# Optimization experiments

Hardware: AMD Instinct MI355X
Metric: run time of the kernel (lower is better)

Reference implementation:

```python
import jax, jax.numpy as jnp
import numpy as np

B, S, D, H = 32, 512, 512, 8
DH = D // H
EXP_FF, EXP_CONV, K = 4, 2, 31
EPS = 1e-5


def _layernorm(x, g, b):
    m = jnp.mean(x, axis=-1, keepdims=True)
    v = jnp.mean(jnp.square(x - m), axis=-1, keepdims=True)
    return (x - m) * jax.lax.rsqrt(v + EPS) * g + b


def _sinusoid_pe(s, d):
    pos = np.arange(s, dtype=np.float32)[:, None]
    i = np.arange(0, d, 2, dtype=np.float32)[None, :]
    ang = pos / np.power(10000.0, i / d)
    pe = np.zeros((s, d), dtype=np.float32)
    pe[:, 0::2] = np.sin(ang)
    pe[:, 1::2] = np.cos(ang)
    return jnp.asarray(pe)


def _rel_shift(ps):
    # Transformer-XL relative shift on [b,h,s,s]
    b, h, s1, s2 = ps.shape
    p = jnp.pad(ps, ((0, 0), (0, 0), (0, 0), (1, 0)))
    p = p.reshape(b, h, s2 + 1, s1)
    return p[:, :, 1:].reshape(b, h, s1, s2)


def setup_inputs() -> dict:
    key = jax.random.key(0)
    ks = iter(jax.random.split(key, 64))
    nrm = lambda shape, sc=0.02: jax.random.normal(next(ks), shape, jnp.float32) * sc
    ones = lambda n: jnp.ones((n,), jnp.float32)
    zeros = lambda n: jnp.zeros((n,), jnp.float32)
    return {
        'x': jax.random.normal(next(ks), (B, S, D), jnp.float32),
        'ff1_g': ones(D), 'ff1_b': zeros(D),
        'ff1_w1': nrm((D, EXP_FF * D)), 'ff1_b1': zeros(EXP_FF * D),
        'ff1_w2': nrm((EXP_FF * D, D)), 'ff1_b2': zeros(D),
        'attn_g': ones(D), 'attn_b': zeros(D),
        'wq': nrm((D, D)), 'bq': zeros(D),
        'wk': nrm((D, D)), 'bk': zeros(D),
        'wv': nrm((D, D)), 'bv': zeros(D),
        'wpos': nrm((D, D)),
        'u_bias': nrm((H, DH)), 'v_bias': nrm((H, DH)),
        'wo': nrm((D, D)), 'bo': zeros(D),
        'conv_g': ones(D), 'conv_b': zeros(D),
        'pw1_w': nrm((D, EXP_CONV * D)), 'pw1_b': zeros(EXP_CONV * D),
        'dw_w': nrm((D, 1, K)),
        'bn_g': ones(D), 'bn_b': zeros(D), 'bn_m': zeros(D), 'bn_v': ones(D),
        'pw2_w': nrm((D, D)), 'pw2_b': zeros(D),
        'ff2_g': ones(D), 'ff2_b': zeros(D),
        'ff2_w1': nrm((D, EXP_FF * D)), 'ff2_b1': zeros(EXP_FF * D),
        'ff2_w2': nrm((EXP_FF * D, D)), 'ff2_b2': zeros(D),
        'ln_g': ones(D), 'ln_b': zeros(D),
    }


def _ff(x, g, b, w1, b1, w2, b2):
    y = _layernorm(x, g, b)
    return jnp.dot(jax.nn.silu(jnp.dot(y, w1) + b1), w2) + b2


def reference(x, ff1_g, ff1_b, ff1_w1, ff1_b1, ff1_w2, ff1_b2,
              attn_g, attn_b, wq, bq, wk, bk, wv, bv, wpos, u_bias, v_bias, wo, bo,
              conv_g, conv_b, pw1_w, pw1_b, dw_w, bn_g, bn_b, bn_m, bn_v, pw2_w, pw2_b,
              ff2_g, ff2_b, ff2_w1, ff2_b1, ff2_w2, ff2_b2, ln_g, ln_b):
    b, s, d = x.shape
    # Macaron FF 1 (half-step residual)
    out = x + 0.5 * _ff(x, ff1_g, ff1_b, ff1_w1, ff1_b1, ff1_w2, ff1_b2)
    # Relative-position multi-head self-attention
    y = _layernorm(out, attn_g, attn_b)
    pe = _sinusoid_pe(s, d)
    q = (jnp.dot(y, wq) + bq).reshape(b, s, H, DH)
    k = (jnp.dot(y, wk) + bk).reshape(b, s, H, DH)
    v = (jnp.dot(y, wv) + bv).reshape(b, s, H, DH)
    p = jnp.dot(pe, wpos).reshape(s, H, DH)
    content = jnp.einsum('bqhd,bkhd->bhqk', q + u_bias, k)
    pos = _rel_shift(jnp.einsum('bqhd,khd->bhqk', q + v_bias, p))
    attn = jax.nn.softmax((content + pos) / np.sqrt(d).astype(np.float32), axis=-1)
    ctx = jnp.einsum('bhqk,bkhd->bqhd', attn, v).reshape(b, s, d)
    out = out + (jnp.dot(ctx, wo) + bo)
    y = _layernorm(out, conv_g, conv_b)
    y = jnp.dot(y, pw1_w) + pw1_b                     # [b,s,2d]
    a, gate = jnp.split(y, 2, axis=-1)
    y = (a * jax.nn.sigmoid(gate)).transpose(0, 2, 1)  # [b,d,s]
    pad = (K - 1) // 2
    y = jax.lax.conv_general_dilated(y, dw_w, (1,), [(pad, pad)],
                                     dimension_numbers=('NCH', 'OIH', 'NCH'),
                                     feature_group_count=d)
    y = (y - bn_m[None, :, None]) * jax.lax.rsqrt(bn_v + EPS)[None, :, None] \
        * bn_g[None, :, None] + bn_b[None, :, None]
    y = jax.nn.silu(y).transpose(0, 2, 1)             # [b,s,d]
    out = out + (jnp.dot(y, pw2_w) + pw2_b)
    # Macaron FF 2 + final LN
    out = out + 0.5 * _ff(out, ff2_g, ff2_b, ff2_w1, ff2_b1, ff2_w2, ff2_b2)
    out = _layernorm(out, ln_g, ln_b)
    return out, attn
```

## Files before the change

### kernel.cpp

```cpp
#include <hip/hip_runtime.h>
#include <cstddef>
#include <cstdint>

#define EPSF 1e-5f

constexpr int BB = 32, SS = 512, DD = 512, HH = 8, DH = 64;
constexpr int NTOK = BB * SS;
constexpr size_t ND = (size_t)NTOK * DD;

typedef __attribute__((ext_vector_type(8))) short bf16x8;
typedef __attribute__((ext_vector_type(4))) float f32x4;

__device__ __forceinline__ float sigmf(float v) { return 1.f / (1.f + __expf(-v)); }

__device__ __forceinline__ ushort f2bf(float f) {
  union { float f; uint32_t u; } x{f};
  uint32_t r = x.u + 0x7FFF + ((x.u >> 16) & 1);
  return (ushort)(r >> 16);
}
__device__ __forceinline__ float bf2f(ushort u) {
  union { uint32_t u; float f; } x{(uint32_t)u << 16};
  return x.f;
}

__device__ __forceinline__ void gload16(const ushort* g, ushort* ldsbase) {
  __builtin_amdgcn_global_load_lds((const __attribute__((address_space(1))) void*)g,
                                   (__attribute__((address_space(3))) void*)ldsbase, 16, 0, 0);
}

__device__ __forceinline__ void xcd_swz(int& bx, int& by) {
  const int gx = gridDim.x;
  const int nwg = gx * gridDim.y;
  const int cpx = nwg >> 3;
  int id = by * gx + bx;
  id = (id & 7) * cpx + (id >> 3);
  bx = id % gx;
  by = id / gx;
}

__global__ __launch_bounds__(256) void ln_f32(const float* __restrict__ x,
                                              const float* __restrict__ g,
                                              const float* __restrict__ b,
                                              float* __restrict__ y) {
  const int lane = threadIdx.x & 63;
  const int row = blockIdx.x * 4 + (threadIdx.x >> 6);
  const float* xr = x + (size_t)row * 512;
  const float4 v0 = *(const float4*)&xr[lane << 2];
  const float4 v1 = *(const float4*)&xr[256 + (lane << 2)];
  float s = v0.x + v0.y + v0.z + v0.w + v1.x + v1.y + v1.z + v1.w;
#pragma unroll
  for (int o = 32; o > 0; o >>= 1) s += __shfl_xor(s, o);
  const float mean = s * (1.f / 512.f);
  float q = 0.f;
  q += (v0.x - mean) * (v0.x - mean); q += (v0.y - mean) * (v0.y - mean);
  q += (v0.z - mean) * (v0.z - mean); q += (v0.w - mean) * (v0.w - mean);
  q += (v1.x - mean) * (v1.x - mean); q += (v1.y - mean) * (v1.y - mean);
  q += (v1.z - mean) * (v1.z - mean); q += (v1.w - mean) * (v1.w - mean);
#pragma unroll
  for (int o = 32; o > 0; o >>= 1) q += __shfl_xor(q, o);
  const float rs = rsqrtf(q * (1.f / 512.f) + EPSF);
  const float4 g0 = *(const float4*)&g[lane << 2];
  const float4 g1 = *(const float4*)&g[256 + (lane << 2)];
  const float4 b0 = *(const float4*)&b[lane << 2];
  const float4 b1 = *(const float4*)&b[256 + (lane << 2)];
  float* yr = y + (size_t)row * 512;
  float4 o0, o1;
  o0.x = (v0.x - mean) * rs * g0.x + b0.x; o0.y = (v0.y - mean) * rs * g0.y + b0.y;
  o0.z = (v0.z - mean) * rs * g0.z + b0.z; o0.w = (v0.w - mean) * rs * g0.w + b0.w;
  o1.x = (v1.x - mean) * rs * g1.x + b1.x; o1.y = (v1.y - mean) * rs * g1.y + b1.y;
  o1.z = (v1.z - mean) * rs * g1.z + b1.z; o1.w = (v1.w - mean) * rs * g1.w + b1.w;
  *(float4*)&yr[lane << 2] = o0;
  *(float4*)&yr[256 + (lane << 2)] = o1;
}

__global__ __launch_bounds__(256) void ln_bf16(const float* __restrict__ x,
                                               const float* __restrict__ g,
                                               const float* __restrict__ b,
                                               ushort* __restrict__ y) {
  const int lane = threadIdx.x & 63;
  const int row = blockIdx.x * 4 + (threadIdx.x >> 6);
  const float* xr = x + (size_t)row * 512;
  const float4 v0 = *(const float4*)&xr[lane << 2];
  const float4 v1 = *(const float4*)&xr[256 + (lane << 2)];
  float s = v0.x + v0.y + v0.z + v0.w + v1.x + v1.y + v1.z + v1.w;
#pragma unroll
  for (int o = 32; o > 0; o >>= 1) s += __shfl_xor(s, o);
  const float mean = s * (1.f / 512.f);
  float q = 0.f;
  q += (v0.x - mean) * (v0.x - mean); q += (v0.y - mean) * (v0.y - mean);
  q += (v0.z - mean) * (v0.z - mean); q += (v0.w - mean) * (v0.w - mean);
  q += (v1.x - mean) * (v1.x - mean); q += (v1.y - mean) * (v1.y - mean);
  q += (v1.z - mean) * (v1.z - mean); q += (v1.w - mean) * (v1.w - mean);
#pragma unroll
  for (int o = 32; o > 0; o >>= 1) q += __shfl_xor(q, o);
  const float rs = rsqrtf(q * (1.f / 512.f) + EPSF);
  const float4 g0 = *(const float4*)&g[lane << 2];
  const float4 g1 = *(const float4*)&g[256 + (lane << 2)];
  const float4 b0 = *(const float4*)&b[lane << 2];
  const float4 b1 = *(const float4*)&b[256 + (lane << 2)];
  ushort* yr = y + (size_t)row * 512;
  ushort4 o0, o1;
  o0.x = f2bf((v0.x - mean) * rs * g0.x + b0.x); o0.y = f2bf((v0.y - mean) * rs * g0.y + b0.y);
  o0.z = f2bf((v0.z - mean) * rs * g0.z + b0.z); o0.w = f2bf((v0.w - mean) * rs * g0.w + b0.w);
  o1.x = f2bf((v1.x - mean) * rs * g1.x + b1.x); o1.y = f2bf((v1.y - mean) * rs * g1.y + b1.y);
  o1.z = f2bf((v1.z - mean) * rs * g1.z + b1.z); o1.w = f2bf((v1.w - mean) * rs * g1.w + b1.w);
  *(ushort4*)&yr[lane << 2] = o0;
  *(ushort4*)&yr[256 + (lane << 2)] = o1;
}

struct TpArgs {
  const float* src[11];
  ushort* dst[11];
  int K[11];
  int N[11];
  int base[12];
};

__global__ __launch_bounds__(256) void transpose_all(TpArgs a) {
  __shared__ float tile[32][33];
  int s = 0;
  const int bid = blockIdx.x;
  while (s < 10 && bid >= a.base[s + 1]) ++s;
  const int r = bid - a.base[s];
  const int K = a.K[s], N = a.N[s];
  const int ntx = N >> 5;
  const int n0 = (r % ntx) << 5;
  const int k0 = (r / ntx) << 5;
  const float* in = a.src[s];
  ushort* out = a.dst[s];
  const int tx = threadIdx.x & 31, ty = threadIdx.x >> 5;
#pragma unroll
  for (int i = 0; i < 32; i += 8)
    tile[ty + i][tx] = in[(size_t)(k0 + ty + i) * N + n0 + tx];
  __syncthreads();
#pragma unroll
  for (int i = 0; i < 32; i += 8)
    out[(size_t)(n0 + ty + i) * K + k0 + tx] = f2bf(tile[tx][ty + i]);
}

template <int ACT, int RES, int HB, int OBF>
__global__ __launch_bounds__(256) void gemm_bf16(const ushort* __restrict__ A,
                                                 const ushort* __restrict__ Wt,
                                                 const float* __restrict__ bias,
                                                 const float* __restrict__ res,
                                                 void* __restrict__ Cv,
                                                 int M, int K, int N) {
  __shared__ ushort Al[2][8192];
  __shared__ ushort Bl[2][8192];
  const int t = threadIdx.x;
  const int lane = t & 63;
  const int w = t >> 6;
  const int wr = (w >> 1) << 6, wc = (w & 1) << 6;
  int bx = blockIdx.x, by = blockIdx.y;
  xcd_swz(bx, by);
  const int m0 = by << 7, n0 = bx << 7;
  const int lm = lane & 15;
  const int grow = lane >> 3;
  const int gcol = (lane & 7) << 3;

  f32x4 acc[4][4];
#pragma unroll
  for (int i = 0; i < 4; ++i)
#pragma unroll
    for (int j = 0; j < 4; ++j) acc[i][j] = (f32x4)(0.f);

  const int NT = K >> 6;
#pragma unroll
  for (int i = 0; i < 4; ++i) {
    const int s = (w << 2) + i;
    gload16(A + (size_t)(m0 + (s << 3) + grow) * K + gcol, &Al[0][s << 9]);
    gload16(Wt + (size_t)(n0 + (s << 3) + grow) * K + gcol, &Bl[0][s << 9]);
  }
  __syncthreads();
  int cur = 0;
  for (int tt = 0; tt < NT; ++tt) {
    if (tt + 1 < NT) {
      const int k0 = (tt + 1) << 6;
#pragma unroll
      for (int i = 0; i < 4; ++i) {
        const int s = (w << 2) + i;
        gload16(A + (size_t)(m0 + (s << 3) + grow) * K + k0 + gcol, &Al[cur ^ 1][s << 9]);
        gload16(Wt + (size_t)(n0 + (s << 3) + grow) * K + k0 + gcol, &Bl[cur ^ 1][s << 9]);
      }
    }
#pragma unroll
    for (int ks = 0; ks < 2; ++ks) {
      const int kof = (ks << 5) + ((lane >> 4) << 3);
      bf16x8 af[4], bfr[4];
#pragma unroll
      for (int i = 0; i < 4; ++i) af[i] = *(const bf16x8*)&Al[cur][(wr + (i << 4) + lm) * 64 + kof];
#pragma unroll
      for (int j = 0; j < 4; ++j) bfr[j] = *(const bf16x8*)&Bl[cur][(wc + (j << 4) + lm) * 64 + kof];
#pragma unroll
      for (int i = 0; i < 4; ++i)
#pragma unroll
        for (int j = 0; j < 4; ++j)
          acc[i][j] = __builtin_amdgcn_mfma_f32_16x16x32_bf16(af[i], bfr[j], acc[i][j], 0, 0, 0);
    }
    __syncthreads();
    cur ^= 1;
  }

  float bb[4] = {0.f, 0.f, 0.f, 0.f};
  if (HB) {
#pragma unroll
    for (int j = 0; j < 4; ++j) bb[j] = bias[n0 + wc + j * 16 + lm];
  }
  const int rbase = m0 + wr + ((lane >> 4) << 2);
#pragma unroll
  for (int i = 0; i < 4; ++i) {
#pragma unroll
    for (int r = 0; r < 4; ++r) {
      const size_t row = (size_t)(rbase + i * 16 + r);
#pragma unroll
      for (int j = 0; j < 4; ++j) {
        const int col = n0 + wc + j * 16 + lm;
        float v = acc[i][j][r] + bb[j];
        if (ACT == 1) v = v * sigmf(v);
        if (RES == 1) v += res[row * N + col];
        else if (RES == 2) v = res[row * N + col] + 0.5f * v;
        if (OBF) ((ushort*)Cv)[row * N + col] = f2bf(v);
        else ((float*)Cv)[row * N + col] = v;
      }
    }
  }
}

__global__ __launch_bounds__(256) void gemm_qkv(const ushort* __restrict__ A,
                                                const ushort* __restrict__ Wt,
                                                const float* __restrict__ bq,
                                                const float* __restrict__ bk,
                                                const float* __restrict__ bv,
                                                const float* __restrict__ ub,
                                                const float* __restrict__ vb,
                                                ushort* __restrict__ qu,
                                                ushort* __restrict__ qv,
                                                ushort* __restrict__ kbb,
                                                ushort* __restrict__ vT,
                                                int M, int K) {
  __shared__ ushort Al[2][8192];
  __shared__ ushort Bl[2][8192];
  const int t = threadIdx.x;
  const int lane = t & 63;
  const int w = t >> 6;
  const int wr = (w >> 1) << 6, wc = (w & 1) << 6;
  int bx = blockIdx.x, by = blockIdx.y;
  xcd_swz(bx, by);
  const int m0 = by << 7, n0 = bx << 7;
  const int lm = lane & 15;
  const int grow = lane >> 3;
  const int gcol = (lane & 7) << 3;
  f32x4 acc[4][4];
#pragma unroll
  for (int i = 0; i < 4; ++i)
#pragma unroll
    for (int j = 0; j < 4; ++j) acc[i][j] = (f32x4)(0.f);
  const int NT = K >> 6;
#pragma unroll
  for (int i = 0; i < 4; ++i) {
    const int s = (w << 2) + i;
    gload16(A + (size_t)(m0 + (s << 3) + grow) * K + gcol, &Al[0][s << 9]);
    gload16(Wt + (size_t)(n0 + (s << 3) + grow) * K + gcol, &Bl[0][s << 9]);
  }
  __syncthreads();
  int cur = 0;
  for (int tt = 0; tt < NT; ++tt) {
    if (tt + 1 < NT) {
      const int k0 = (tt + 1) << 6;
#pragma unroll
      for (int i = 0; i < 4; ++i) {
        const int s = (w << 2) + i;
        gload16(A + (size_t)(m0 + (s << 3) + grow) * K + k0 + gcol, &Al[cur ^ 1][s << 9]);
        gload16(Wt + (size_t)(n0 + (s << 3) + grow) * K + k0 + gcol, &Bl[cur ^ 1][s << 9]);
      }
    }
#pragma unroll
    for (int ks = 0; ks < 2; ++ks) {
      const int kof = (ks << 5) + ((lane >> 4) << 3);
      bf16x8 af[4], bfr[4];
#pragma unroll
      for (int i = 0; i < 4; ++i) af[i] = *(const bf16x8*)&Al[cur][(wr + (i << 4) + lm) * 64 + kof];
#pragma unroll
      for (int j = 0; j < 4; ++j) bfr[j] = *(const bf16x8*)&Bl[cur][(wc + (j << 4) + lm) * 64 + kof];
#pragma unroll
      for (int i = 0; i < 4; ++i)
#pragma unroll
        for (int j = 0; j < 4; ++j)
          acc[i][j] = __builtin_amdgcn_mfma_f32_16x16x32_bf16(af[i], bfr[j], acc[i][j], 0, 0, 0);
    }
    __syncthreads();
    cur ^= 1;
  }
  const int seg = n0 >> 9;
  const int nloc = n0 & 511;
  const float* bsel = (seg == 0) ? bq : (seg == 1 ? bk : bv);
  float bb[4], uu[4], vv[4];
#pragma unroll
  for (int j = 0; j < 4; ++j) {
    const int col = nloc + wc + j * 16 + lm;
    bb[j] = bsel[col];
    if (seg == 0) { uu[j] = ub[col]; vv[j] = vb[col]; }
  }
  const int rbase = m0 + wr + ((lane >> 4) << 2);
  if (seg == 2) {
    const int bloc = m0 >> 9;
    const int sbase = rbase - (bloc << 9);
#pragma unroll
    for (int i = 0; i < 4; ++i) {
#pragma unroll
      for (int j = 0; j < 4; ++j) {
        const int col = nloc + wc + j * 16 + lm;
        ushort4 o;
        o.x = f2bf(acc[i][j][0] + bb[j]);
        o.y = f2bf(acc[i][j][1] + bb[j]);
        o.z = f2bf(acc[i][j][2] + bb[j]);
        o.w = f2bf(acc[i][j][3] + bb[j]);
        *(ushort4*)&vT[((size_t)((bloc << 9) + col)) * 512 + sbase + i * 16] = o;
      }
    }
    return;
  }
#pragma unroll
  for (int i = 0; i < 4; ++i) {
#pragma unroll
    for (int r = 0; r < 4; ++r) {
      const size_t row = (size_t)(rbase + i * 16 + r);
#pragma unroll
      for (int j = 0; j < 4; ++j) {
        const int col = nloc + wc + j * 16 + lm;
        const float v = acc[i][j][r] + bb[j];
        if (seg == 0) {
          qu[row * 512 + col] = f2bf(v + uu[j]);
          qv[row * 512 + col] = f2bf(v + vv[j]);
        } else {
          kbb[row * 512 + col] = f2bf(v);
        }
      }
    }
  }
}

__global__ __launch_bounds__(256) void gemm_glu(const ushort* __restrict__ A,
                                                const ushort* __restrict__ Wt,
                                                const float* __restrict__ bias,
                                                ushort* __restrict__ Cout,
                                                int M, int K) {
  __shared__ ushort Al[8192];
  __shared__ ushort Ba[8192];
  __shared__ ushort Bg[8192];
  const int t = threadIdx.x;
  const int lane = t & 63;
  const int w = t >> 6;
  const int wr = (w >> 1) << 6, wc = (w & 1) << 6;
  int bx = blockIdx.x, by = blockIdx.y;
  xcd_swz(bx, by);
  const int m0 = by << 7, n0 = bx << 7;
  const int lm = lane & 15;
  const int grow = lane >> 3;
  const int gcol = (lane & 7) << 3;
  const ushort* WtA = Wt;
  const ushort* WtG = Wt + (size_t)512 * 512;
  f32x4 acca[4][4], accg[4][4];
#pragma unroll
  for (int i = 0; i < 4; ++i)
#pragma unroll
    for (int j = 0; j < 4; ++j) { acca[i][j] = (f32x4)(0.f); accg[i][j] = (f32x4)(0.f); }
  const int NT = K >> 6;
  for (int tt = 0; tt < NT; ++tt) {
    const int k0 = tt << 6;
    if (tt) __syncthreads();
#pragma unroll
    for (int i = 0; i < 4; ++i) {
      const int s = (w << 2) + i;
      gload16(A + (size_t)(m0 + (s << 3) + grow) * K + k0 + gcol, &Al[s << 9]);
      gload16(WtA + (size_t)(n0 + (s << 3) + grow) * K + k0 + gcol, &Ba[s << 9]);
      gload16(WtG + (size_t)(n0 + (s << 3) + grow) * K + k0 + gcol, &Bg[s << 9]);
    }
    __syncthreads();
#pragma unroll
    for (int ks = 0; ks < 2; ++ks) {
      const int kof = (ks << 5) + ((lane >> 4) << 3);
      bf16x8 af[4], ba4[4], bg4[4];
#pragma unroll
      for (int i = 0; i < 4; ++i) af[i] = *(const bf16x8*)&Al[(wr + (i << 4) + lm) * 64 + kof];
#pragma unroll
      for (int j = 0; j < 4; ++j) {
        ba4[j] = *(const bf16x8*)&Ba[(wc + (j << 4) + lm) * 64 + kof];
        bg4[j] = *(const bf16x8*)&Bg[(wc + (j << 4) + lm) * 64 + kof];
      }
#pragma unroll
      for (int i = 0; i < 4; ++i)
#pragma unroll
        for (int j = 0; j < 4; ++j) {
          acca[i][j] = __builtin_amdgcn_mfma_f32_16x16x32_bf16(af[i], ba4[j], acca[i][j], 0, 0, 0);
          accg[i][j] = __builtin_amdgcn_mfma_f32_16x16x32_bf16(af[i], bg4[j], accg[i][j], 0, 0, 0);
        }
    }
  }
  float bba[4], bbg[4];
#pragma unroll
  for (int j = 0; j < 4; ++j) {
    const int col = n0 + wc + j * 16 + lm;
    bba[j] = bias[col];
    bbg[j] = bias[512 + col];
  }
  const int rbase = m0 + wr + ((lane >> 4) << 2);
#pragma unroll
  for (int i = 0; i < 4; ++i) {
#pragma unroll
    for (int r = 0; r < 4; ++r) {
      const size_t row = (size_t)(rbase + i * 16 + r);
#pragma unroll
      for (int j = 0; j < 4; ++j) {
        const int col = n0 + wc + j * 16 + lm;
        const float va = acca[i][j][r] + bba[j];
        const float vg = accg[i][j][r] + bbg[j];
        Cout[row * 512 + col] = f2bf(va * sigmf(vg));
      }
    }
  }
}

__global__ void pe_kernel_bf16(ushort* __restrict__ pe) {
  const int pos = blockIdx.x, ii = threadIdx.x;
  const float ang = (float)pos * powf(10000.f, -(float)(2 * ii) / 512.f);
  pe[((size_t)pos << 9) + 2 * ii] = f2bf(sinf(ang));
  pe[((size_t)pos << 9) + 2 * ii + 1] = f2bf(cosf(ang));
}

__global__ __launch_bounds__(256, 3) void attn_fused7(const ushort* __restrict__ qu,
                                                      const ushort* __restrict__ qv,
                                                      const ushort* __restrict__ kbb,
                                                      const ushort* __restrict__ ppb,
                                                      const ushort* __restrict__ vT,
                                                      float* __restrict__ attn,
                                                      ushort* __restrict__ ctx) {
  __shared__ ushort psL[33][520];
  __shared__ union StU {
    struct { ushort p[2][32][72]; ushort k[2][32][72]; } pk;
    ushort v2[2][64][40];
    float scr[4][32];
    float scrC[2][64][16];
  } su;
  const int t = threadIdx.x, lane = t & 63, w = t >> 6;
  int bx = blockIdx.x, by = blockIdx.y;
  xcd_swz(bx, by);
  const int z = by, b = z >> 3, hh = z & 7;
  const int q0 = bx << 5;
  const int band = w >> 1, half = w & 1;
  const int lm = lane & 15, g = lane >> 4;
  const int lk = g << 3, fr4 = g << 2;
  const int C0 = half << 8;

  const size_t qoff = ((size_t)((b << 9) + q0 + (band << 4) + lm)) * 512 + (hh << 6);
  const bf16x8 av0 = *(const bf16x8*)&qv[qoff + lk];
  const bf16x8 av1 = *(const bf16x8*)&qv[qoff + lk + 32];
  const bf16x8 au0 = *(const bf16x8*)&qu[qoff + lk];
  const bf16x8 au1 = *(const bf16x8*)&qu[qoff + lk + 32];
  int er = q0 + 32 + lm;
  if (er > 511) er = 511;
  const size_t eoff = ((size_t)((b << 9) + er)) * 512 + (hh << 6);
  const bf16x8 e0 = *(const bf16x8*)&qv[eoff + lk];
  const bf16x8 e1 = *(const bf16x8*)&qv[eoff + lk + 32];

  const int srow = t >> 2, scg = (t & 3) << 4;
  const int sh = srow >> 5, sr = srow & 31;

  f32x4 acc[16];
#pragma unroll
  for (int i = 0; i < 16; ++i) acc[i] = (f32x4)(0.f);
  {
    const ushort* pb_ = ppb + (hh << 6);
    const ushort* kb_ = kbb + ((size_t)(b << 9)) * 512 + (hh << 6);
    const size_t off0 = (size_t)((sh << 8) + sr) * 512 + scg;
    bf16x8 rp0 = *(const bf16x8*)&pb_[off0];
    bf16x8 rp1 = *(const bf16x8*)&pb_[off0 + 8];
    bf16x8 rk0 = *(const bf16x8*)&kb_[off0];
    bf16x8 rk1 = *(const bf16x8*)&kb_[off0 + 8];
#pragma unroll
    for (int it = 0; it < 8; ++it) {
      __syncthreads();
      *(bf16x8*)&su.pk.p[sh][sr][scg] = rp0;
      *(bf16x8*)&su.pk.p[sh][sr][scg + 8] = rp1;
      *(bf16x8*)&su.pk.k[sh][sr][scg] = rk0;
      *(bf16x8*)&su.pk.k[sh][sr][scg + 8] = rk1;
      if (it < 7) {
        const size_t off = (size_t)((sh << 8) + ((it + 1) << 5) + sr) * 512 + scg;
        rp0 = *(const bf16x8*)&pb_[off];
        rp1 = *(const bf16x8*)&pb_[off + 8];
        rk0 = *(const bf16x8*)&kb_[off];
        rk1 = *(const bf16x8*)&kb_[off + 8];
      }
      __syncthreads();
#pragma unroll
      for (int ctl = 0; ctl < 2; ++ctl) {
        {
          const bf16x8 b0 = *(const bf16x8*)&su.pk.p[half][(ctl << 4) + lm][lk];
          const bf16x8 b1 = *(const bf16x8*)&su.pk.p[half][(ctl << 4) + lm][32 + lk];
          f32x4 a = (f32x4)(0.f);
          a = __builtin_amdgcn_mfma_f32_16x16x32_bf16(av0, b0, a, 0, 0, 0);
          a = __builtin_amdgcn_mfma_f32_16x16x32_bf16(av1, b1, a, 0, 0, 0);
          const int col = C0 + (it << 5) + (ctl << 4) + lm;
#pragma unroll
          for (int r = 0; r < 4; ++r) psL[(band << 4) + fr4 + r][col] = f2bf(a[r]);
          if (ctl == band) {
            f32x4 e = (f32x4)(0.f);
            e = __builtin_amdgcn_mfma_f32_16x16x32_bf16(e0, b0, e, 0, 0, 0);
            e = __builtin_amdgcn_mfma_f32_16x16x32_bf16(e1, b1, e, 0, 0, 0);
            if (g == 0) psL[32][col] = f2bf(e[0]);
          }
        }
        {
          const int lct = (it << 1) + ctl;
          const bf16x8 b0 = *(const bf16x8*)&su.pk.k[half][(ctl << 4) + lm][lk];
          const bf16x8 b1 = *(const bf16x8*)&su.pk.k[half][(ctl << 4) + lm][32 + lk];
          acc[lct] = __builtin_amdgcn_mfma_f32_16x16x32_bf16(au0, b0, acc[lct], 0, 0, 0);
          acc[lct] = __builtin_amdgcn_mfma_f32_16x16x32_bf16(au1, b1, acc[lct], 0, 0, 0);
        }
      }
    }
  }
  __syncthreads();

  const float scale = 0.044194173824159216f;
  const int qq0 = (band << 4) + fr4;
#pragma unroll
  for (int lct = 0; lct < 16; ++lct) {
#pragma unroll
    for (int r = 0; r < 4; ++r) {
      const int qq = qq0 + r;
      const int q = q0 + qq;
      const int c = C0 + (lct << 4) + lm;
      float f;
      if (c <= q)          f = bf2f(psL[qq][c - q + 511]);
      else if (c == q + 1) f = 0.f;
      else                 f = bf2f(psL[qq + 1][c - q - 2]);
      acc[lct][r] = (acc[lct][r] + f) * scale;
    }
  }

  float mx[4] = {-3.0e38f, -3.0e38f, -3.0e38f, -3.0e38f};
#pragma unroll
  for (int lct = 0; lct < 16; ++lct)
#pragma unroll
    for (int r = 0; r < 4; ++r) mx[r] = fmaxf(mx[r], acc[lct][r]);
#pragma unroll
  for (int o = 1; o < 16; o <<= 1)
#pragma unroll
    for (int r = 0; r < 4; ++r) mx[r] = fmaxf(mx[r], __shfl_xor(mx[r], o));
  if (lm == 0) {
#pragma unroll
    for (int r = 0; r < 4; ++r) su.scr[half][qq0 + r] = mx[r];
  }
  __syncthreads();
#pragma unroll
  for (int r = 0; r < 4; ++r) mx[r] = fmaxf(mx[r], su.scr[half ^ 1][qq0 + r]);
  float sme[4] = {0.f, 0.f, 0.f, 0.f};
#pragma unroll
  for (int lct = 0; lct < 16; ++lct)
#pragma unroll
    for (int r = 0; r < 4; ++r) {
      acc[lct][r] = __expf(acc[lct][r] - mx[r]);
      sme[r] += acc[lct][r];
    }
#pragma unroll
  for (int o = 1; o < 16; o <<= 1)
#pragma unroll
    for (int r = 0; r < 4; ++r) sme[r] += __shfl_xor(sme[r], o);
  if (lm == 0) {
#pragma unroll
    for (int r = 0; r < 4; ++r) su.scr[2 + half][qq0 + r] = sme[r];
  }
  __syncthreads();
#pragma unroll
  for (int r = 0; r < 4; ++r) {
    const float inv = 1.f / (sme[r] + su.scr[2 + (half ^ 1)][qq0 + r]);
#pragma unroll
    for (int lct = 0; lct < 16; ++lct) acc[lct][r] *= inv;
  }
  __syncthreads();

  ushort* Pl = (ushort*)&psL[0][0] + ((band << 1) | half) * 704;
  const ushort* vtb = vT + ((size_t)((b << 9) + (hh << 6))) * 512;
  const int vrow = t >> 1, vc = (t & 1) << 4;
  const int vh = vrow >> 6, vd = vrow & 63;
  float* abase = attn + ((size_t)z << 18);
  f32x4 acc2[4];
#pragma unroll
  for (int i = 0; i < 4; ++i) acc2[i] = (f32x4)(0.f);
  bf16x8 p0 = *(const bf16x8*)&vtb[(size_t)vd * 512 + (vh << 8) + vc];
  bf16x8 p1 = *(const bf16x8*)&vtb[(size_t)vd * 512 + (vh << 8) + vc + 8];
#pragma unroll
  for (int ch = 0; ch < 8; ++ch) {
#pragma unroll
    for (int ctl = 0; ctl < 2; ++ctl) {
      const int lct = (ch << 1) + ctl;
#pragma unroll
      for (int r = 0; r < 4; ++r)
        Pl[(fr4 + r) * 44 + (ctl << 4) + lm] = f2bf(acc[lct][r]);
    }
    __syncthreads();
    *(bf16x8*)&su.v2[vh][vd][vc] = p0;
    *(bf16x8*)&su.v2[vh][vd][vc + 8] = p1;
    if (ch < 7) {
      const size_t off = (size_t)vd * 512 + (vh << 8) + ((ch + 1) << 5) + vc;
      p0 = *(const bf16x8*)&vtb[off];
      p1 = *(const bf16x8*)&vtb[off + 8];
    }
    {
      const int row = lane >> 2, colg = (lane & 3) << 3;
      const ushort* ps = Pl + row * 44 + colg;
      float* ar = abase + (size_t)(q0 + (band << 4) + row) * 512 + C0 + (ch << 5) + colg;
      float4 o0, o1;
      o0.x = bf2f(ps[0]); o0.y = bf2f(ps[1]); o0.z = bf2f(ps[2]); o0.w = bf2f(ps[3]);
      o1.x = bf2f(ps[4]); o1.y = bf2f(ps[5]); o1.z = bf2f(ps[6]); o1.w = bf2f(ps[7]);
      *(float4*)&ar[0] = o0;
      *(float4*)&ar[4] = o1;
    }
    __syncthreads();
#pragma unroll
    for (int dt = 0; dt < 4; ++dt) {
      const bf16x8 va = *(const bf16x8*)&su.v2[half][(dt << 4) + lm][lk];
      const bf16x8 pbf = *(const bf16x8*)&Pl[lm * 44 + lk];
      acc2[dt] = __builtin_amdgcn_mfma_f32_16x16x32_bf16(va, pbf, acc2[dt], 0, 0, 0);
    }
  }
  __syncthreads();
  if (half == 1) {
#pragma unroll
    for (int dt = 0; dt < 4; ++dt)
#pragma unroll
      for (int r = 0; r < 4; ++r)
        su.scrC[band][(dt << 4) + fr4 + r][lm] = acc2[dt][r];
  }
  __syncthreads();
  if (half == 0) {
    const int qq2 = q0 + (band << 4) + lm;
#pragma unroll
    for (int dt = 0; dt < 4; ++dt) {
      ushort4 o;
      o.x = f2bf(acc2[dt][0] + su.scrC[band][(dt << 4) + fr4 + 0][lm]);
      o.y = f2bf(acc2[dt][1] + su.scrC[band][(dt << 4) + fr4 + 1][lm]);
      o.z = f2bf(acc2[dt][2] + su.scrC[band][(dt << 4) + fr4 + 2][lm]);
      o.w = f2bf(acc2[dt][3] + su.scrC[band][(dt << 4) + fr4 + 3][lm]);
      *(ushort4*)&ctx[((size_t)((b << 9) + qq2)) * 512 + (hh << 6) + (dt << 4) + fr4] = o;
    }
  }
}

__global__ __launch_bounds__(256) void dwconv2(const ushort* __restrict__ in,
                                               const float* __restrict__ w,
                                               const float* __restrict__ bng,
                                               const float* __restrict__ bnb,
                                               const float* __restrict__ bnm,
                                               const float* __restrict__ bnv,
                                               ushort* __restrict__ out) {
  __shared__ float wl[31][128];
  const int t = threadIdx.x;
  const int dbase = blockIdx.x << 7;
  const int b = blockIdx.z;
  const int sb = (blockIdx.y << 6) + ((t >> 6) << 4);
  if (t < 128) {
    const float* ws = &w[(dbase + t) * 31];
#pragma unroll
    for (int k = 0; k < 31; ++k) wl[k][t] = ws[k];
  }
  __syncthreads();
  const int dl = (t & 63) << 1;
  const int d = dbase + dl;
  const size_t base = (((size_t)b) << 18) + d;
  float2 win[46];
#pragma unroll
  for (int i = 0; i < 46; ++i) {
    const int s = sb - 15 + i;
    if (s >= 0 && s < 512) {
      const ushort2 u = *(const ushort2*)&in[base + ((size_t)s << 9)];
      win[i].x = bf2f(u.x); win[i].y = bf2f(u.y);
    } else {
      win[i].x = 0.f; win[i].y = 0.f;
    }
  }
  float2 acc[16];
#pragma unroll
  for (int p = 0; p < 16; ++p) { acc[p].x = 0.f; acc[p].y = 0.f; }
#pragma unroll
  for (int k = 0; k < 31; ++k) {
    const float2 w2 = *(const float2*)&wl[k][dl];
#pragma unroll
    for (int p = 0; p < 16; ++p) {
      acc[p].x = fmaf(win[p + k].x, w2.x, acc[p].x);
      acc[p].y = fmaf(win[p + k].y, w2.y, acc[p].y);
    }
  }
  const float g0 = bng[d] * rsqrtf(bnv[d] + EPSF);
  const float g1 = bng[d + 1] * rsqrtf(bnv[d + 1] + EPSF);
  const float m0 = bnm[d], m1 = bnm[d + 1];
  const float bb0 = bnb[d], bb1 = bnb[d + 1];
#pragma unroll
  for (int p = 0; p < 16; ++p) {
    float v0 = (acc[p].x - m0) * g0 + bb0;
    float v1 = (acc[p].y - m1) * g1 + bb1;
    v0 = v0 * sigmf(v0);
    v1 = v1 * sigmf(v1);
    ushort2 o;
    o.x = f2bf(v0); o.y = f2bf(v1);
    *(ushort2*)&out[base + ((size_t)(sb + p) << 9)] = o;
  }
}

extern "C" void kernel_launch(void* const* d_in, const int* in_sizes, int n_in,
                              void* d_out, int out_size, void* d_ws, size_t ws_size,
                              hipStream_t stream) {
  const float* x      = (const float*)d_in[0];
  const float* ff1_g  = (const float*)d_in[1];
  const float* ff1_b  = (const float*)d_in[2];
  const float* ff1_w1 = (const float*)d_in[3];
  const float* ff1_b1 = (const float*)d_in[4];
  const float* ff1_w2 = (const float*)d_in[5];
  const float* ff1_b2 = (const float*)d_in[6];
  const float* attn_g = (const float*)d_in[7];
  const float* attn_b = (const float*)d_in[8];
  const float* wq     = (const float*)d_in[9];
  const float* bq     = (const float*)d_in[10];
  const float* wk     = (const float*)d_in[11];
  const float* bk     = (const float*)d_in[12];
  const float* wv     = (const float*)d_in[13];
  const float* bv     = (const float*)d_in[14];
  const float* wpos   = (const float*)d_in[15];
  const float* u_bias = (const float*)d_in[16];
  const float* v_bias = (const float*)d_in[17];
  const float* wo     = (const float*)d_in[18];
  const float* bo     = (const float*)d_in[19];
  const float* conv_g = (const float*)d_in[20];
  const float* conv_b = (const float*)d_in[21];
  const float* pw1_w  = (const float*)d_in[22];
  const float* pw1_b  = (const float*)d_in[23];
  const float* dw_w   = (const float*)d_in[24];
  const float* bn_g   = (const float*)d_in[25];
  const float* bn_b   = (const float*)d_in[26];
  const float* bn_m   = (const float*)d_in[27];
  const float* bn_v   = (const float*)d_in[28];
  const float* pw2_w  = (const float*)d_in[29];
  const float* pw2_b  = (const float*)d_in[30];
  const float* ff2_g  = (const float*)d_in[31];
  const float* ff2_b  = (const float*)d_in[32];
  const float* ff2_w1 = (const float*)d_in[33];
  const float* ff2_b1 = (const float*)d_in[34];
  const float* ff2_w2 = (const float*)d_in[35];
  const float* ff2_b2 = (const float*)d_in[36];
  const float* ln_g   = (const float*)d_in[37];
  const float* ln_b   = (const float*)d_in[38];

  float* out  = (float*)d_out;
  float* attn = out + ND;

  float*  res  = (float*)d_ws;
  ushort* ybf  = (ushort*)(res + ND);
  float*  big  = (float*)(ybf + ND);
  ushort* vT   = (ushort*)(big + 2 * ND);
  ushort* dwbf = vT + ND;
  ushort* wts  = dwbf + ND;
  ushort* pebf = wts + 6291456;
  ushort* ppbf = pebf + 262144;

  ushort* ffmid = (ushort*)big;
  ushort* qu    = (ushort*)big;
  ushort* qv    = qu + ND;
  ushort* kbb   = qv + ND;
  ushort* ctxbf = ybf;
  ushort* glubf = (ushort*)big;

  ushort* ff1w1t = wts;
  ushort* ff1w2t = wts + 1048576;
  ushort* wqt    = wts + 2097152;
  ushort* wkt    = wts + 2359296;
  ushort* wvt    = wts + 2621440;
  ushort* wot    = wts + 2883584;
  ushort* pw1t   = wts + 3145728;
  ushort* pw2t   = wts + 3670016;
  ushort* ff2w1t = wts + 3932160;
  ushort* ff2w2t = wts + 4980736;
  ushort* wpost  = wts + 6029312;

  const dim3 blk(256);

  TpArgs ta;
  auto set = [&](int i, const float* s, ushort* d, int K, int N) {
    ta.src[i] = s; ta.dst[i] = d; ta.K[i] = K; ta.N[i] = N;
  };
  set(0, ff1_w1, ff1w1t, 512, 2048);
  set(1, ff1_w2, ff1w2t, 2048, 512);
  set(2, wq, wqt, 512, 512);
  set(3, wk, wkt, 512, 512);
  set(4, wv, wvt, 512, 512);
  set(5, wo, wot, 512, 512);
  set(6, wpos, wpost, 512, 512);
  set(7, pw1_w, pw1t, 512, 1024);
  set(8, pw2_w, pw2t, 512, 512);
  set(9, ff2_w1, ff2w1t, 512, 2048);
  set(10, ff2_w2, ff2w2t, 2048, 512);
  int tacc = 0;
  for (int i = 0; i < 11; ++i) { ta.base[i] = tacc; tacc += (ta.N[i] >> 5) * (ta.K[i] >> 5); }
  ta.base[11] = tacc;
  transpose_all<<<tacc, blk, 0, stream>>>(ta);
  pe_kernel_bf16<<<512, blk, 0, stream>>>(pebf);
  gemm_bf16<0, 0, 0, 1><<<dim3(4, 4), blk, 0, stream>>>(pebf, wpost, nullptr, nullptr, ppbf,
                                                        512, 512, 512);

  ln_bf16<<<NTOK / 4, blk, 0, stream>>>(x, ff1_g, ff1_b, ybf);
  gemm_bf16<1, 0, 1, 1><<<dim3(16, 128), blk, 0, stream>>>(ybf, ff1w1t, ff1_b1, nullptr, ffmid,
                                                           NTOK, 512, 2048);
  gemm_bf16<0, 2, 1, 0><<<dim3(4, 128), blk, 0, stream>>>(ffmid, ff1w2t, ff1_b2, x, res,
                                                          NTOK, 2048, 512);

  ln_bf16<<<NTOK / 4, blk, 0, stream>>>(res, attn_g, attn_b, ybf);
  gemm_qkv<<<dim3(12, 128), blk, 0, stream>>>(ybf, wqt, bq, bk, bv, u_bias, v_bias,
                                              qu, qv, kbb, vT, NTOK, 512);
  attn_fused7<<<dim3(16, 256), blk, 0, stream>>>(qu, qv, kbb, ppbf, vT, attn, ctxbf);
  gemm_bf16<0, 1, 1, 0><<<dim3(4, 128), blk, 0, stream>>>(ctxbf, wot, bo, res, res,
                                                          NTOK, 512, 512);

  ln_bf16<<<NTOK / 4, blk, 0, stream>>>(res, conv_g, conv_b, ybf);
  gemm_glu<<<dim3(4, 128), blk, 0, stream>>>(ybf, pw1t, pw1_b, glubf, NTOK, 512);
  dwconv2<<<dim3(4, 8, 32), blk, 0, stream>>>(glubf, dw_w, bn_g, bn_b, bn_m, bn_v, dwbf);
  gemm_bf16<0, 1, 1, 0><<<dim3(4, 128), blk, 0, stream>>>(dwbf, pw2t, pw2_b, res, res,
                                                          NTOK, 512, 512);

  ln_bf16<<<NTOK / 4, blk, 0, stream>>>(res, ff2_g, ff2_b, ybf);
  gemm_bf16<1, 0, 1, 1><<<dim3(16, 128), blk, 0, stream>>>(ybf, ff2w1t, ff2_b1, nullptr, ffmid,
                                                           NTOK, 512, 2048);
  gemm_bf16<0, 2, 1, 0><<<dim3(4, 128), blk, 0, stream>>>(ffmid, ff2w2t, ff2_b2, res, res,
                                                          NTOK, 2048, 512);
  ln_f32<<<NTOK / 4, blk, 0, stream>>>(res, ln_g, ln_b, out);
}
```

Before: 730.4 us.

## Linearize relative-shift LDS buffer with swizzle and branchless gather in attention

Flattens the position-score LDS buffer to a 513-stride linear array with an XOR swizzle and a pre-zeroed gap slot. This turns the three-way Transformer-XL rel-shift branch into one contiguous indexed load. It also pads the P staging and scrC scratch strides to reduce LDS bank conflicts, and raises wave priority around the MFMA sections. The swizzle and padding add index arithmetic, and the buffer grows slightly, which could affect occupancy at 3 blocks per CU.

```diff
diff --git a/kernel.cpp b/kernel.cpp
--- a/kernel.cpp
+++ b/kernel.cpp
@@ -36,6 +36,10 @@
   id = (id & 7) * cpx + (id >> 3);
   bx = id % gx;
   by = id / gx;
+}
+
+__device__ __forceinline__ int pswz(int idx) {
+  return idx ^ (((idx >> 11) & 3) << 4);
 }
 
 __global__ __launch_bounds__(256) void ln_f32(const float* __restrict__ x,
@@ -428,19 +432,19 @@
   pe[((size_t)pos << 9) + 2 * ii + 1] = f2bf(cosf(ang));
 }
 
-__global__ __launch_bounds__(256, 3) void attn_fused7(const ushort* __restrict__ qu,
+__global__ __launch_bounds__(256, 3) void attn_fused8(const ushort* __restrict__ qu,
                                                       const ushort* __restrict__ qv,
                                                       const ushort* __restrict__ kbb,
                                                       const ushort* __restrict__ ppb,
                                                       const ushort* __restrict__ vT,
                                                       float* __restrict__ attn,
                                                       ushort* __restrict__ ctx) {
-  __shared__ ushort psL[33][520];
+  __shared__ ushort psl[17024];
   __shared__ union StU {
     struct { ushort p[2][32][72]; ushort k[2][32][72]; } pk;
     ushort v2[2][64][40];
     float scr[4][32];
-    float scrC[2][64][16];
+    float scrC[2][64][17];
   } su;
   const int t = threadIdx.x, lane = t & 63, w = t >> 6;
   int bx = blockIdx.x, by = blockIdx.y;
@@ -451,6 +455,11 @@
   const int lm = lane & 15, g = lane >> 4;
   const int lk = g << 3, fr4 = g << 2;
   const int C0 = half << 8;
+
+  if (t < 33) {
+    const int zi = t * 513 + 512;
+    psl[pswz(zi)] = 0;
+  }
 
   const size_t qoff = ((size_t)((b << 9) + q0 + (band << 4) + lm)) * 512 + (hh << 6);
   const bf16x8 av0 = *(const bf16x8*)&qv[qoff + lk];
@@ -492,6 +501,7 @@
         rk1 = *(const bf16x8*)&kb_[off + 8];
       }
       __syncthreads();
+      __builtin_amdgcn_s_setprio(1);
 #pragma unroll
       for (int ctl = 0; ctl < 2; ++ctl) {
         {
@@ -502,12 +512,18 @@
           a = __builtin_amdgcn_mfma_f32_16x16x32_bf16(av1, b1, a, 0, 0, 0);
           const int col = C0 + (it << 5) + (ctl << 4) + lm;
 #pragma unroll
-          for (int r = 0; r < 4; ++r) psL[(band << 4) + fr4 + r][col] = f2bf(a[r]);
+          for (int r = 0; r < 4; ++r) {
+            const int idx = ((band << 4) + fr4 + r) * 513 + col;
+            psl[pswz(idx)] = f2bf(a[r]);
+          }
           if (ctl == band) {
             f32x4 e = (f32x4)(0.f);
             e = __builtin_amdgcn_mfma_f32_16x16x32_bf16(e0, b0, e, 0, 0, 0);
             e = __builtin_amdgcn_mfma_f32_16x16x32_bf16(e1, b1, e, 0, 0, 0);
-            if (g == 0) psL[32][col] = f2bf(e[0]);
+            if (g == 0) {
+              const int idx = 32 * 513 + col;
+              psl[pswz(idx)] = f2bf(e[0]);
+            }
           }
         }
         {
@@ -518,6 +534,7 @@
           acc[lct] = __builtin_amdgcn_mfma_f32_16x16x32_bf16(au1, b1, acc[lct], 0, 0, 0);
         }
       }
+      __builtin_amdgcn_s_setprio(0);
     }
   }
   __syncthreads();
@@ -525,16 +542,12 @@
   const float scale = 0.044194173824159216f;
   const int qq0 = (band << 4) + fr4;
 #pragma unroll
-  for (int lct = 0; lct < 16; ++lct) {
-#pragma unroll
-    for (int r = 0; r < 4; ++r) {
-      const int qq = qq0 + r;
-      const int q = q0 + qq;
-      const int c = C0 + (lct << 4) + lm;
-      float f;
-      if (c <= q)          f = bf2f(psL[qq][c - q + 511]);
-      else if (c == q + 1) f = 0.f;
-      else                 f = bf2f(psL[qq + 1][c - q - 2]);
+  for (int r = 0; r < 4; ++r) {
+    const int qq = qq0 + r;
+    const int pbase = qq * 512 + 511 - q0 + C0 + lm;
+#pragma unroll
+    for (int lct = 0; lct < 16; ++lct) {
+      const float f = bf2f(psl[pswz(pbase + (lct << 4))]);
       acc[lct][r] = (acc[lct][r] + f) * scale;
     }
   }
@@ -580,7 +593,7 @@
   }
   __syncthreads();
 
-  ushort* Pl = (ushort*)&psL[0][0] + ((band << 1) | half) * 704;
+  ushort* Pl = psl + ((band << 1) | half) * 736;
   const ushort* vtb = vT + ((size_t)((b << 9) + (hh << 6))) * 512;
   const int vrow = t >> 1, vc = (t & 1) << 4;
   const int vh = vrow >> 6, vd = vrow & 63;
@@ -597,7 +610,7 @@
       const int lct = (ch << 1) + ctl;
 #pragma unroll
       for (int r = 0; r < 4; ++r)
-        Pl[(fr4 + r) * 44 + (ctl << 4) + lm] = f2bf(acc[lct][r]);
+        Pl[(fr4 + r) * 46 + (ctl << 4) + lm] = f2bf(acc[lct][r]);
     }
     __syncthreads();
     *(bf16x8*)&su.v2[vh][vd][vc] = p0;
@@ -609,7 +622,7 @@
     }
     {
       const int row = lane >> 2, colg = (lane & 3) << 3;
-      const ushort* ps = Pl + row * 44 + colg;
+      const ushort* ps = Pl + row * 46 + colg;
       float* ar = abase + (size_t)(q0 + (band << 4) + row) * 512 + C0 + (ch << 5) + colg;
       float4 o0, o1;
       o0.x = bf2f(ps[0]); o0.y = bf2f(ps[1]); o0.z = bf2f(ps[2]); o0.w = bf2f(ps[3]);
@@ -618,12 +631,14 @@
       *(float4*)&ar[4] = o1;
     }
     __syncthreads();
+    __builtin_amdgcn_s_setprio(1);
 #pragma unroll
     for (int dt = 0; dt < 4; ++dt) {
       const bf16x8 va = *(const bf16x8*)&su.v2[half][(dt << 4) + lm][lk];
-      const bf16x8 pbf = *(const bf16x8*)&Pl[lm * 44 + lk];
+      const bf16x8 pbf = *(const bf16x8*)&Pl[lm * 46 + lk];
       acc2[dt] = __builtin_amdgcn_mfma_f32_16x16x32_bf16(va, pbf, acc2[dt], 0, 0, 0);
     }
+    __builtin_amdgcn_s_setprio(0);
   }
   __syncthreads();
   if (half == 1) {
@@ -816,7 +831,7 @@
   ln_bf16<<<NTOK / 4, blk, 0, stream>>>(res, attn_g, attn_b, ybf);
   gemm_qkv<<<dim3(12, 128), blk, 0, stream>>>(ybf, wqt, bq, bk, bv, u_bias, v_bias,
                                               qu, qv, kbb, vT, NTOK, 512);
-  attn_fused7<<<dim3(16, 256), blk, 0, stream>>>(qu, qv, kbb, ppbf, vT, attn, ctxbf);
+  attn_fused8<<<dim3(16, 256), blk, 0, stream>>>(qu, qv, kbb, ppbf, vT, attn, ctxbf);
   gemm_bf16<0, 1, 1, 0><<<dim3(4, 128), blk, 0, stream>>>(ctxbf, wot, bo, res, res,
                                                           NTOK, 512, 512);
 
```

Result: no change. 718.6 us (-1.6%).
